# Kernel optimization log

Measured on AMD Instinct MI355X. Metric: run time of the kernel, lower is better.

Reference implementation:

```python
import jax, jax.numpy as jnp
import numpy as np

B, T, D, H = 1, 2048, 1024, 16
HS = D // H  # 64
FF = 4 * D   # 4096
EPS = 1e-6


def rmsnorm(x, w):
    xf = x.astype(jnp.float32)
    n = xf * jax.lax.rsqrt(jnp.mean(xf * xf, axis=-1, keepdims=True) + EPS)
    return n.astype(x.dtype) * w


def setup_inputs() -> dict:
    key = jax.random.key(0)
    ks = jax.random.split(key, 9)
    s = 0.02
    return {
        "x": jax.random.normal(ks[0], (B, T, D), jnp.float32),
        "Wq": jax.random.normal(ks[1], (H, D, HS), jnp.float32) * s,
        "Wk": jax.random.normal(ks[2], (H, D, HS), jnp.float32) * s,
        "Wv": jax.random.normal(ks[3], (H, D, HS), jnp.float32) * s,
        "Wproj": jax.random.normal(ks[4], (H * HS, D), jnp.float32) * s,
        "bproj": jnp.zeros((D,), jnp.float32),
        "W1": jax.random.normal(ks[5], (D, FF), jnp.float32) * s,
        "W2": jax.random.normal(ks[6], (FF, D), jnp.float32) * s,
        "g1": jnp.ones((D,), jnp.float32),
        "g2": jnp.ones((D,), jnp.float32),
    }


def reference(x, Wq, Wk, Wv, Wproj, bproj, W1, W2, g1, g2):
    # --- self attention on RMSNorm(x) ---
    xn = rmsnorm(x, g1)                                   # [B,T,D]
    q = jnp.einsum('btd,hds->bhts', xn, Wq)               # [B,H,T,hs]
    k = jnp.einsum('btd,hds->bhts', xn, Wk)
    v = jnp.einsum('btd,hds->bhts', xn, Wv)
    scale = HS ** -0.5
    wei = jnp.einsum('bhts,bhus->bhtu', q, k) * scale     # [B,H,T,T]
    causal = jnp.tril(jnp.ones((T, T), bool))
    wei = jnp.where(causal, wei, -jnp.inf)
    wei = jax.nn.softmax(wei, axis=-1)
    attn = jnp.einsum('bhtu,bhus->bhts', wei, v)          # [B,H,T,hs]
    attn = attn.transpose(0, 2, 1, 3).reshape(B, T, H * HS)
    sa = attn @ Wproj + bproj                             # [B,T,D]
    x = x + sa
    # --- SiLU FFN on RMSNorm(x) ---
    xn2 = rmsnorm(x, g2)
    h = jax.nn.silu(xn2 @ W1)                             # [B,T,4D]
    x = x + h @ W2
    return x
```

## Files before the change

### kernel.cpp

```cpp
#include <hip/hip_runtime.h>

typedef unsigned short u16;
typedef unsigned int u32;
typedef __attribute__((ext_vector_type(4))) float f32x4;
typedef __attribute__((ext_vector_type(8))) __bf16 bf16x8;

#define T_SEQ 2048
#define DMODEL 1024
#define NHEAD 16
#define HEADS 64
#define FFDIM 4096
#define MNQ 2097152l

__device__ __forceinline__ u16 f2bf(float f) {
  u32 u = __builtin_bit_cast(u32, f);
  u = u + 0x7FFFu + ((u >> 16) & 1u);
  return (u16)(u >> 16);
}
__device__ __forceinline__ float bf2f(u16 h) {
  u32 u = ((u32)h) << 16;
  return __builtin_bit_cast(float, u);
}
__device__ __forceinline__ void gload_lds16(const u16* g, u16* l) {
  __builtin_amdgcn_global_load_lds(
      (const __attribute__((address_space(1))) u32*)g,
      (__attribute__((address_space(3))) u32*)l, 16, 0, 0);
}

__device__ __forceinline__ void transpose64(const float* __restrict__ in,
                                            long ldin, u16* __restrict__ out,
                                            long ldout, int r0, int c0, int tid,
                                            u16* tile) {
#pragma unroll
  for (int p = 0; p < 4; ++p) {
    int idx = p * 256 + tid;
    int r = idx >> 4, c4 = (idx & 15) * 4;
    float4 v = *(const float4*)(in + (long)(r0 + r) * ldin + c0 + c4);
    tile[(c4 + 0) * 66 + r] = f2bf(v.x);
    tile[(c4 + 1) * 66 + r] = f2bf(v.y);
    tile[(c4 + 2) * 66 + r] = f2bf(v.z);
    tile[(c4 + 3) * 66 + r] = f2bf(v.w);
  }
  __syncthreads();
#pragma unroll
  for (int p = 0; p < 2; ++p) {
    int idx = p * 256 + tid;
    int c = idx >> 3, rg = (idx & 7) * 8;
    u16 tmp[8];
#pragma unroll
    for (int j = 0; j < 8; ++j) tmp[j] = tile[c * 66 + rg + j];
    *(uint4*)(out + (long)(c0 + c) * ldout + r0 + rg) = *(uint4*)tmp;
  }
}

__global__ __launch_bounds__(256) void prep_k(
    const float* __restrict__ Wq, const float* __restrict__ Wk,
    const float* __restrict__ Wv, const float* __restrict__ Wproj,
    const float* __restrict__ x, const float* __restrict__ g1,
    u16* __restrict__ QKVwT, u16* __restrict__ WprojT, u16* __restrict__ xn1) {
  __shared__ u16 tile[64 * 66];
  __shared__ float wsum[4];
  int bid = blockIdx.x;
  int tid = threadIdx.x;
  if (bid >= 1024) {
    int row = bid - 1024;
    const float4* xr = (const float4*)(x + (long)row * DMODEL);
    float4 v = xr[tid];
    float ss = v.x * v.x + v.y * v.y + v.z * v.z + v.w * v.w;
#pragma unroll
    for (int off = 32; off >= 1; off >>= 1) ss += __shfl_xor(ss, off, 64);
    if ((tid & 63) == 0) wsum[tid >> 6] = ss;
    __syncthreads();
    float tot = wsum[0] + wsum[1] + wsum[2] + wsum[3];
    float rms = rsqrtf(tot * (1.0f / DMODEL) + 1e-6f);
    float4 gv = ((const float4*)g1)[tid];
    ushort4 o4 = make_ushort4(f2bf(v.x * rms * gv.x), f2bf(v.y * rms * gv.y),
                              f2bf(v.z * rms * gv.z), f2bf(v.w * rms * gv.w));
    ((ushort4*)(xn1 + (long)row * DMODEL))[tid] = o4;
    return;
  }
  const float* in;
  u16* out;
  long ldin, ldout;
  int r0, c0;
  if (bid < 768) {
    int z = bid >> 4, xi = bid & 15;
    int wsel = z >> 4, h = z & 15;
    in = (wsel == 0 ? Wq : (wsel == 1 ? Wk : Wv)) + (long)h * 65536;
    out = QKVwT + (long)wsel * 1048576 + (long)h * 65536;
    ldin = 64; ldout = 1024;
    r0 = xi * 64; c0 = 0;
  } else {
    int b = bid - 768;
    in = Wproj; out = WprojT; ldin = 1024; ldout = 1024;
    r0 = (b >> 4) * 64; c0 = (b & 15) * 64;
  }
  transpose64(in, ldin, out, ldout, r0, c0, tid, tile);
}

__global__ __launch_bounds__(256) void proj_rms_k(
    const u16* __restrict__ part, const float* __restrict__ bias,
    const float* __restrict__ resid, const float* __restrict__ g,
    float* __restrict__ x1, u16* __restrict__ xn2) {
  int row = blockIdx.x;
  int tid = threadIdx.x;
  long i = (long)row * DMODEL + tid * 4;
  float4 r = *(const float4*)(resid + i);
  float4 bi = *(const float4*)(bias + tid * 4);
  float4 v;
  v.x = r.x + bi.x; v.y = r.y + bi.y; v.z = r.z + bi.z; v.w = r.w + bi.w;
#pragma unroll
  for (int z = 0; z < 2; ++z) {
    ushort4 a = *(const ushort4*)(part + z * MNQ + i);
    v.x += bf2f(a.x); v.y += bf2f(a.y); v.z += bf2f(a.z); v.w += bf2f(a.w);
  }
  *(float4*)(x1 + i) = v;
  float ss = v.x * v.x + v.y * v.y + v.z * v.z + v.w * v.w;
#pragma unroll
  for (int off = 32; off >= 1; off >>= 1) ss += __shfl_xor(ss, off, 64);
  __shared__ float wsum[4];
  if ((tid & 63) == 0) wsum[tid >> 6] = ss;
  __syncthreads();
  float tot = wsum[0] + wsum[1] + wsum[2] + wsum[3];
  float rms = rsqrtf(tot * (1.0f / DMODEL) + 1e-6f);
  float4 gv = ((const float4*)g)[tid];
  ushort4 o4 = make_ushort4(f2bf(v.x * rms * gv.x), f2bf(v.y * rms * gv.y),
                            f2bf(v.z * rms * gv.z), f2bf(v.w * rms * gv.w));
  ((ushort4*)(xn2 + (long)row * DMODEL))[tid] = o4;
}

template <int EPI, int MODE, int NITER, bool FILL = false>
__global__ __launch_bounds__(256, 3) void gemm_bt_k(
    const u16* __restrict__ A, const u16* __restrict__ Bt, int N,
    u16* __restrict__ out16, u16* __restrict__ vt,
    u16* __restrict__ p0, u16* __restrict__ p1,
    const float* __restrict__ F1, const float* __restrict__ F2,
    u16* __restrict__ FT1, u16* __restrict__ FT2, int ngemm) {
  __shared__ __align__(16) u16 As[3][128 * 32];
  __shared__ __align__(16) u16 Bs[3][128 * 32];
  if constexpr (FILL) {
    if ((int)blockIdx.x >= ngemm) {
      int tb = (int)blockIdx.x - ngemm;
      u16* tile = (u16*)As;
      const float* in;
      u16* out;
      long ldin, ldout;
      int r0, c0;
      if (tb < 1024) {
        in = F1; out = FT1; ldin = 4096; ldout = 1024;
        r0 = (tb & 15) * 64; c0 = (tb >> 4) * 64;
      } else {
        int b = tb - 1024;
        in = F2; out = FT2; ldin = 1024; ldout = 4096;
        r0 = (b >> 4) * 64; c0 = (b & 15) * 64;
      }
      transpose64(in, ldin, out, ldout, r0, c0, threadIdx.x, tile);
      return;
    }
  }
  const int K = 1024;
  const int kc = NITER * 32;
  int tid = threadIdx.x;
  int w = tid >> 6, lane = tid & 63;
  int quad = lane >> 4, l15 = lane & 15;
  int wr = w >> 1, wc = w & 1;

  int bid = blockIdx.x;
  int xcd = bid & 7, s = bid >> 3;
  int nn = N >> 7;
  int bx, by, kz;
  {
    int nl = nn >> 3;
    by = xcd * nl + s % nl;
    int r = s / nl;
    bx = r & 15;
    kz = r >> 4;
  }
  int m0 = bx * 128, n0 = by * 128;

  f32x4 acc[4][4] = {};

  int lr = lane >> 2;
  int sw = (lr >> 1) & 3;
  int lc = ((lane & 3) ^ sw) * 8;
  const u16* Ak = A + (long)(m0 + w * 32 + lr) * K + lc + (long)kz * kc;
  const u16* A2k = Ak + (long)16 * K;
  const u16* Bk = Bt + (long)(n0 + w * 32 + lr) * K + lc + (long)kz * kc;
  const u16* B2k = Bk + (long)16 * K;

  gload_lds16(Ak, As[0] + w * 1024);
  gload_lds16(A2k, As[0] + w * 1024 + 512);
  gload_lds16(Bk, Bs[0] + w * 1024);
  gload_lds16(B2k, Bs[0] + w * 1024 + 512);
  gload_lds16(Ak + 32, As[1] + w * 1024);
  gload_lds16(A2k + 32, As[1] + w * 1024 + 512);
  gload_lds16(Bk + 32, Bs[1] + w * 1024);
  gload_lds16(B2k + 32, Bs[1] + w * 1024 + 512);

  int swq = (l15 >> 1) & 3;
  int qoff = (quad ^ swq) << 3;

#pragma unroll
  for (int k = 0; k < NITER; ++k) {
    const int cb = k % 3;
    if (k + 2 < NITER) {
      asm volatile("s_waitcnt vmcnt(4)\n\ts_barrier" ::: "memory");
      const int pb = (k + 2) % 3;
      const int off = (k + 2) * 32;
      gload_lds16(Ak + off, As[pb] + w * 1024);
      gload_lds16(A2k + off, As[pb] + w * 1024 + 512);
      gload_lds16(Bk + off, Bs[pb] + w * 1024);
      gload_lds16(B2k + off, Bs[pb] + w * 1024 + 512);
    } else {
      asm volatile("s_waitcnt vmcnt(0)\n\ts_barrier" ::: "memory");
    }
    const u16* Ab = As[cb];
    const u16* Bb = Bs[cb];
    bf16x8 af[4], bfr[4];
#pragma unroll
    for (int mt = 0; mt < 4; ++mt)
      af[mt] = *(const bf16x8*)(Ab + (wr * 64 + mt * 16 + l15) * 32 + qoff);
#pragma unroll
    for (int nt = 0; nt < 4; ++nt)
      bfr[nt] = *(const bf16x8*)(Bb + (wc * 64 + nt * 16 + l15) * 32 + qoff);
#pragma unroll
    for (int mt = 0; mt < 4; ++mt)
#pragma unroll
      for (int nt = 0; nt < 4; ++nt)
        acc[mt][nt] = __builtin_amdgcn_mfma_f32_16x16x32_bf16(
            af[mt], bfr[nt], acc[mt][nt], 0, 0, 0);
  }

  bool vblock = (EPI == 0) && (vt != nullptr) && (n0 >= 2048);
  u16* pb = nullptr;
  if (EPI == 4) pb = p0 + (long)kz * MNQ;
#pragma unroll
  for (int mt = 0; mt < 4; ++mt)
#pragma unroll
    for (int nt = 0; nt < 4; ++nt) {
      int col = n0 + wc * 64 + nt * 16 + l15;
      if (EPI == 0 && vblock) {
        int sc = col - 2048;
        int row0 = m0 + wr * 64 + mt * 16 + quad * 4;
        ushort4 pk = make_ushort4(f2bf(acc[mt][nt][0]), f2bf(acc[mt][nt][1]),
                                  f2bf(acc[mt][nt][2]), f2bf(acc[mt][nt][3]));
        *(ushort4*)(vt + (long)sc * 2048 + row0) = pk;
        continue;
      }
#pragma unroll
      for (int r = 0; r < 4; ++r) {
        int row = m0 + wr * 64 + mt * 16 + quad * 4 + r;
        long idx = (long)row * N + col;
        float v = acc[mt][nt][r];
        if (EPI == 0) {
          out16[idx] = f2bf(v);
        } else if (EPI == 4) {
          pb[idx] = f2bf(v);
        }
      }
    }
}

template <int EPI, int NITER>
__global__ __launch_bounds__(256, 2) void gemm_wide_k(
    const u16* __restrict__ A, const u16* __restrict__ Bt,
    u16* __restrict__ out16, u16* __restrict__ p0, u16* __restrict__ p1) {
  __shared__ __align__(16) u16 As[3][128 * 32];
  __shared__ __align__(16) u16 Bs[3][256 * 32];
  const int K = (EPI == 4) ? 4096 : 1024;
  const int N = (EPI == 4) ? 1024 : 4096;
  const int kc = NITER * 32;
  int tid = threadIdx.x;
  int w = tid >> 6, lane = tid & 63;
  int quad = lane >> 4, l15 = lane & 15;
  int wr = w >> 1, wc = w & 1;

  int bid = blockIdx.x;
  int xcd = bid & 7, s = bid >> 3;
  int bx, by, kz;
  if (EPI == 2) {
    by = xcd * 2 + (s & 1);
    bx = s >> 1;
    kz = 0;
  } else {
    kz = xcd;
    by = s & 3;
    bx = s >> 2;
  }
  int m0 = bx * 128, n0 = by * 256;

  f32x4 acc[4][8] = {};

  int lr = lane >> 2;
  int sw = (lr >> 1) & 3;
  int lc = ((lane & 3) ^ sw) * 8;
  const u16* Ak = A + (long)(m0 + w * 32 + lr) * K + (long)kz * kc + lc;
  const u16* A2k = Ak + (long)16 * K;
  const u16* Bk0 = Bt + (long)(n0 + w * 64 + lr) * K + (long)kz * kc + lc;
  const u16* Bk1 = Bk0 + (long)16 * K;
  const u16* Bk2 = Bk0 + (long)32 * K;
  const u16* Bk3 = Bk0 + (long)48 * K;

#pragma unroll
  for (int t = 0; t < 2; ++t) {
    const int off = t * 32;
    gload_lds16(Ak + off, As[t] + w * 1024);
    gload_lds16(A2k + off, As[t] + w * 1024 + 512);
    gload_lds16(Bk0 + off, Bs[t] + w * 2048);
    gload_lds16(Bk1 + off, Bs[t] + w * 2048 + 512);
    gload_lds16(Bk2 + off, Bs[t] + w * 2048 + 1024);
    gload_lds16(Bk3 + off, Bs[t] + w * 2048 + 1536);
  }

  int swq = (l15 >> 1) & 3;
  int qoff = (quad ^ swq) << 3;

#pragma unroll
  for (int k = 0; k < NITER; ++k) {
    const int cb = k % 3;
    if (k + 2 < NITER) {
      asm volatile("s_waitcnt vmcnt(6)\n\ts_barrier" ::: "memory");
      const int pb2 = (k + 2) % 3;
      const int off = (k + 2) * 32;
      gload_lds16(Ak + off, As[pb2] + w * 1024);
      gload_lds16(A2k + off, As[pb2] + w * 1024 + 512);
      gload_lds16(Bk0 + off, Bs[pb2] + w * 2048);
      gload_lds16(Bk1 + off, Bs[pb2] + w * 2048 + 512);
      gload_lds16(Bk2 + off, Bs[pb2] + w * 2048 + 1024);
      gload_lds16(Bk3 + off, Bs[pb2] + w * 2048 + 1536);
    } else if (k + 2 == NITER) {
      asm volatile("s_waitcnt vmcnt(6)\n\ts_barrier" ::: "memory");
    } else {
      asm volatile("s_waitcnt vmcnt(0)\n\ts_barrier" ::: "memory");
    }
    const u16* Ab = As[cb];
    const u16* Bb = Bs[cb];
    bf16x8 af[4], bfr[8];
#pragma unroll
    for (int mt = 0; mt < 4; ++mt)
      af[mt] = *(const bf16x8*)(Ab + (wr * 64 + mt * 16 + l15) * 32 + qoff);
#pragma unroll
    for (int nt = 0; nt < 8; ++nt)
      bfr[nt] = *(const bf16x8*)(Bb + (wc * 128 + nt * 16 + l15) * 32 + qoff);
#pragma unroll
    for (int mt = 0; mt < 4; ++mt)
#pragma unroll
      for (int nt = 0; nt < 8; ++nt)
        acc[mt][nt] = __builtin_amdgcn_mfma_f32_16x16x32_bf16(
            af[mt], bfr[nt], acc[mt][nt], 0, 0, 0);
  }

  u16* pb = nullptr;
  if (EPI == 4)
    pb = (kz < 4) ? (p0 + (long)kz * MNQ) : (p1 + (long)(kz - 4) * MNQ);
#pragma unroll
  for (int mt = 0; mt < 4; ++mt)
#pragma unroll
    for (int nt = 0; nt < 8; ++nt) {
      int col = n0 + wc * 128 + nt * 16 + l15;
#pragma unroll
      for (int r = 0; r < 4; ++r) {
        int row = m0 + wr * 64 + mt * 16 + quad * 4 + r;
        float v = acc[mt][nt][r];
        if (EPI == 2) {
          out16[(long)row * N + col] = f2bf(v / (1.0f + __expf(-v)));
        } else {
          pb[(long)row * N + col] = f2bf(v);
        }
      }
    }
}

__global__ __launch_bounds__(256) void reduce_ffn2_k(
    const u16* __restrict__ p0, const u16* __restrict__ p1,
    const float* __restrict__ resid, float* __restrict__ out) {
  long i = ((long)blockIdx.x * 256 + threadIdx.x) * 4;
  float4 r = *(const float4*)(resid + i);
  float4 o = r;
#pragma unroll
  for (int z = 0; z < 4; ++z) {
    ushort4 a = *(const ushort4*)(p0 + z * MNQ + i);
    ushort4 b = *(const ushort4*)(p1 + z * MNQ + i);
    o.x += bf2f(a.x) + bf2f(b.x);
    o.y += bf2f(a.y) + bf2f(b.y);
    o.z += bf2f(a.z) + bf2f(b.z);
    o.w += bf2f(a.w) + bf2f(b.w);
  }
  *(float4*)(out + i) = o;
}

#define LSTR 72
__global__ __launch_bounds__(256) void attn_part_k(const u16* __restrict__ QKV,
                                                   const u16* __restrict__ Vt,
                                                   u16* __restrict__ Opart,
                                                   float* __restrict__ lpart,
                                                   u16* __restrict__ attn) {
  __shared__ __align__(16) u16 Qs[64 * LSTR];
  __shared__ __align__(16) u16 Ks[64 * LSTR];
  __shared__ __align__(16) u16 Vs[64 * LSTR];
  __shared__ float lbuf[64];

  int tid = threadIdx.x;
  int w = tid >> 6, lane = tid & 63;
  int quad = lane >> 4, l15 = lane & 15;

  int bid = blockIdx.x;
  int xcd = bid & 7, sg = bid >> 3;
  int h = xcd * 2 + (sg & 1);
  int p = sg >> 1;

  int bx = 0, acc0 = 0;
  while (true) {
    int n = (bx >> 3) + 1;
    if (p < acc0 + n) break;
    acc0 += n;
    ++bx;
  }
  int c = p - acc0;
  int t0 = bx * 64;
  int jstart = c * 8;
  int jend = min(jstart + 8, bx + 1);

#pragma unroll
  for (int pp = 0; pp < 2; ++pp) {
    int idx = pp * 256 + tid;
    int row = idx >> 3, cc = idx & 7;
    *(uint4*)(Qs + row * LSTR + cc * 8) =
        *(const uint4*)(QKV + (long)(t0 + row) * 3072 + h * 64 + cc * 8);
  }
  __syncthreads();
  bf16x8 aq[2];
#pragma unroll
  for (int ks = 0; ks < 2; ++ks)
    aq[ks] = *(const bf16x8*)(Qs + (w * 16 + l15) * LSTR + ks * 32 + quad * 8);

  f32x4 oacc[4] = {};
  float lsum = 0.f;
  int qg = t0 + w * 16 + l15;

  u16* PsW = Qs + w * (16 * LSTR);

  for (int j = jstart; j < jend; ++j) {
    __syncthreads();
#pragma unroll
    for (int pp = 0; pp < 2; ++pp) {
      int idx = pp * 256 + tid;
      int row = idx >> 3, cc = idx & 7;
      *(uint4*)(Ks + row * LSTR + cc * 8) =
          *(const uint4*)(QKV + (long)(j * 64 + row) * 3072 + 1024 + h * 64 + cc * 8);
      *(uint4*)(Vs + row * LSTR + cc * 8) =
          *(const uint4*)(Vt + (long)h * (64 * 2048) + (long)row * 2048 + j * 64 + cc * 8);
    }
    __syncthreads();

    f32x4 sacc[4] = {};
#pragma unroll
    for (int ks = 0; ks < 2; ++ks)
#pragma unroll
      for (int ut = 0; ut < 4; ++ut) {
        bf16x8 kf = *(const bf16x8*)(Ks + (ut * 16 + l15) * LSTR + ks * 32 + quad * 8);
        sacc[ut] = __builtin_amdgcn_mfma_f32_16x16x32_bf16(kf, aq[ks], sacc[ut], 0, 0, 0);
      }

    bool boundary = (j == bx);
#pragma unroll
    for (int ut = 0; ut < 4; ++ut) {
      float pv[4];
#pragma unroll
      for (int r = 0; r < 4; ++r) {
        float v = exp2f(sacc[ut][r] * 0.18033688f);
        if (boundary) {
          int u = j * 64 + ut * 16 + quad * 4 + r;
          if (u > qg) v = 0.f;
        }
        pv[r] = v;
        lsum += v;
      }
      ushort4 pk = make_ushort4(f2bf(pv[0]), f2bf(pv[1]), f2bf(pv[2]), f2bf(pv[3]));
      *(ushort4*)(PsW + l15 * LSTR + ut * 16 + quad * 4) = pk;
    }
    asm volatile("s_waitcnt lgkmcnt(0)" ::: "memory");
#pragma unroll
    for (int ks = 0; ks < 2; ++ks) {
      bf16x8 pf = *(const bf16x8*)(PsW + l15 * LSTR + ks * 32 + quad * 8);
#pragma unroll
      for (int ct = 0; ct < 4; ++ct) {
        bf16x8 vf = *(const bf16x8*)(Vs + (ct * 16 + l15) * LSTR + ks * 32 + quad * 8);
        oacc[ct] = __builtin_amdgcn_mfma_f32_16x16x32_bf16(pf, vf, oacc[ct], 0, 0, 0);
      }
    }
  }

  lsum += __shfl_xor(lsum, 16, 64);
  lsum += __shfl_xor(lsum, 32, 64);
  if (quad == 0) lbuf[w * 16 + l15] = 1.0f / lsum;
  asm volatile("s_waitcnt lgkmcnt(0)" ::: "memory");

  float inv[4];
#pragma unroll
  for (int r = 0; r < 4; ++r) inv[r] = lbuf[w * 16 + quad * 4 + r];

  if (bx < 8) {
#pragma unroll
    for (int ct = 0; ct < 4; ++ct)
#pragma unroll
      for (int r = 0; r < 4; ++r)
        attn[(long)(t0 + w * 16 + quad * 4 + r) * 1024 + h * 64 + ct * 16 + l15] =
            f2bf(oacc[ct][r] * inv[r]);
    return;
  }
  long slot = (long)p * 16 + h;
  u16* Ob = Opart + slot * 4096;
#pragma unroll
  for (int ct = 0; ct < 4; ++ct)
#pragma unroll
    for (int r = 0; r < 4; ++r)
      Ob[(w * 16 + quad * 4 + r) * 64 + ct * 16 + l15] = f2bf(oacc[ct][r] * inv[r]);
  if (quad == 0) lpart[slot * 64 + w * 16 + l15] = lsum;
}

__global__ __launch_bounds__(256) void attn_combine_k(
    const u16* __restrict__ Opart, const float* __restrict__ lpart,
    u16* __restrict__ out) {
  int bx = blockIdx.x + 8, h = blockIdx.y;
  int g = bx >> 3;
  int p0 = 4 * g * (g + 1) + (bx - 8 * g) * (g + 1);
  int nc = g + 1;
  int tid = threadIdx.x;
  int row = tid >> 2, c4 = (tid & 3) * 16;

  float lv[4];
  float wsum = 0.f;
  for (int cidx = 0; cidx < nc; ++cidx) {
    long slot = (long)(p0 + cidx) * 16 + h;
    lv[cidx] = lpart[slot * 64 + row];
    wsum += lv[cidx];
  }
  float rinv = 1.0f / wsum;

  float o[16];
#pragma unroll
  for (int i = 0; i < 16; ++i) o[i] = 0.f;
  for (int cidx = 0; cidx < nc; ++cidx) {
    float wc = lv[cidx] * rinv;
    const u16* Ob = Opart + ((long)(p0 + cidx) * 16 + h) * 4096 + row * 64 + c4;
    bf16x8 a = *(const bf16x8*)Ob;
    bf16x8 b = *(const bf16x8*)(Ob + 8);
#pragma unroll
    for (int i = 0; i < 8; ++i) {
      o[i] += wc * (float)a[i];
      o[8 + i] += wc * (float)b[i];
    }
  }
  u16 ob[16];
#pragma unroll
  for (int i = 0; i < 16; ++i) ob[i] = f2bf(o[i]);
  u16* op = out + (long)(bx * 64 + row) * 1024 + h * 64 + c4;
  *(uint4*)op = *(uint4*)ob;
  *(uint4*)(op + 8) = *(uint4*)(ob + 8);
}

extern "C" void kernel_launch(void* const* d_in, const int* in_sizes, int n_in,
                              void* d_out, int out_size, void* d_ws, size_t ws_size,
                              hipStream_t stream) {
  const float* x     = (const float*)d_in[0];
  const float* Wq    = (const float*)d_in[1];
  const float* Wk    = (const float*)d_in[2];
  const float* Wv    = (const float*)d_in[3];
  const float* Wproj = (const float*)d_in[4];
  const float* bproj = (const float*)d_in[5];
  const float* W1    = (const float*)d_in[6];
  const float* W2    = (const float*)d_in[7];
  const float* g1    = (const float*)d_in[8];
  const float* g2    = (const float*)d_in[9];

  char* ws = (char*)d_ws;
  u16* QKVwT  = (u16*)(ws);
  u16* WprojT = (u16*)(ws + (6ul << 20));
  u16* W1T    = (u16*)(ws + (8ul << 20));
  u16* W2T    = (u16*)(ws + (16ul << 20));
  u16* xn1    = (u16*)(ws + (24ul << 20));
  u16* QKVb   = (u16*)(ws + (28ul << 20));
  u16* VtB    = (u16*)(ws + (40ul << 20));
  u16* attn   = (u16*)(ws + (44ul << 20));
  float* x1   = (float*)(ws + (48ul << 20));
  u16* xn2    = (u16*)(ws + (56ul << 20));
  u16* hbuf   = (u16*)(ws + (60ul << 20));
  u16* Opart    = (u16*)(ws + (48ul << 20));
  float* lpart  = (float*)(ws + (58ul << 20));
  u16* projp    = (u16*)(ws + (28ul << 20));
  u16* ffn2pA   = (u16*)(ws + (28ul << 20));
  u16* ffn2pB   = (u16*)(ws);
  if (ws_size < (76ul << 20)) return;

  dim3 blk(256);

  prep_k<<<dim3(3072), blk, 0, stream>>>(
      Wq, Wk, Wv, Wproj, x, g1, QKVwT, WprojT, xn1);
  gemm_bt_k<0, 0, 32, true><<<dim3(2432), blk, 0, stream>>>(
      xn1, QKVwT, 3072, QKVb, VtB, nullptr, nullptr, W1, W2, W1T, W2T, 384);
  attn_part_k<<<dim3(1280), blk, 0, stream>>>(QKVb, VtB, Opart, lpart, attn);
  attn_combine_k<<<dim3(24, 16), blk, 0, stream>>>(Opart, lpart, attn);
  gemm_bt_k<4, 0, 16><<<dim3(256), blk, 0, stream>>>(
      attn, WprojT, 1024, nullptr, nullptr, projp, nullptr,
      nullptr, nullptr, nullptr, nullptr, 0);
  proj_rms_k<<<dim3(2048), blk, 0, stream>>>(projp, bproj, x, g2, x1, xn2);
  gemm_wide_k<2, 32><<<dim3(256), blk, 0, stream>>>(
      xn2, W1T, hbuf, nullptr, nullptr);
  gemm_wide_k<4, 16><<<dim3(512), blk, 0, stream>>>(
      hbuf, W2T, nullptr, ffn2pA, ffn2pB);
  reduce_ffn2_k<<<dim3(2048), blk, 0, stream>>>(ffn2pA, ffn2pB, x1, (float*)d_out);
}
```

Before: 243.8 us.

## Move Wproj transpose into QKV fill, prefetch attention K/V, split proj GEMM 4-way

Moves the Wproj transpose out of the prep kernel and into the fill blocks of the QKV GEMM, so it overlaps with GEMM work and the prep grid shrinks. The attention kernel now loads the next K/V tile into registers while computing the current one, hiding global load latency at the cost of extra registers. The projection GEMM uses a smaller K chunk with twice the blocks (4-way split-K), and the proj_rms reduction sums 4 partials. The extra partials add memory traffic in exchange for more parallelism.

```diff
diff --git a/kernel.cpp b/kernel.cpp
--- a/kernel.cpp
+++ b/kernel.cpp
@@ -55,15 +55,15 @@
 
 __global__ __launch_bounds__(256) void prep_k(
     const float* __restrict__ Wq, const float* __restrict__ Wk,
-    const float* __restrict__ Wv, const float* __restrict__ Wproj,
-    const float* __restrict__ x, const float* __restrict__ g1,
-    u16* __restrict__ QKVwT, u16* __restrict__ WprojT, u16* __restrict__ xn1) {
+    const float* __restrict__ Wv, const float* __restrict__ x,
+    const float* __restrict__ g1, u16* __restrict__ QKVwT,
+    u16* __restrict__ xn1) {
   __shared__ u16 tile[64 * 66];
   __shared__ float wsum[4];
   int bid = blockIdx.x;
   int tid = threadIdx.x;
-  if (bid >= 1024) {
-    int row = bid - 1024;
+  if (bid >= 768) {
+    int row = bid - 768;
     const float4* xr = (const float4*)(x + (long)row * DMODEL);
     float4 v = xr[tid];
     float ss = v.x * v.x + v.y * v.y + v.z * v.z + v.w * v.w;
@@ -79,23 +79,11 @@
     ((ushort4*)(xn1 + (long)row * DMODEL))[tid] = o4;
     return;
   }
-  const float* in;
-  u16* out;
-  long ldin, ldout;
-  int r0, c0;
-  if (bid < 768) {
-    int z = bid >> 4, xi = bid & 15;
-    int wsel = z >> 4, h = z & 15;
-    in = (wsel == 0 ? Wq : (wsel == 1 ? Wk : Wv)) + (long)h * 65536;
-    out = QKVwT + (long)wsel * 1048576 + (long)h * 65536;
-    ldin = 64; ldout = 1024;
-    r0 = xi * 64; c0 = 0;
-  } else {
-    int b = bid - 768;
-    in = Wproj; out = WprojT; ldin = 1024; ldout = 1024;
-    r0 = (b >> 4) * 64; c0 = (b & 15) * 64;
-  }
-  transpose64(in, ldin, out, ldout, r0, c0, tid, tile);
+  int z = bid >> 4, xi = bid & 15;
+  int wsel = z >> 4, h = z & 15;
+  const float* in = (wsel == 0 ? Wq : (wsel == 1 ? Wk : Wv)) + (long)h * 65536;
+  u16* out = QKVwT + (long)wsel * 1048576 + (long)h * 65536;
+  transpose64(in, 64, out, 1024, xi * 64, 0, tid, tile);
 }
 
 __global__ __launch_bounds__(256) void proj_rms_k(
@@ -110,7 +98,7 @@
   float4 v;
   v.x = r.x + bi.x; v.y = r.y + bi.y; v.z = r.z + bi.z; v.w = r.w + bi.w;
 #pragma unroll
-  for (int z = 0; z < 2; ++z) {
+  for (int z = 0; z < 4; ++z) {
     ushort4 a = *(const ushort4*)(part + z * MNQ + i);
     v.x += bf2f(a.x); v.y += bf2f(a.y); v.z += bf2f(a.z); v.w += bf2f(a.w);
   }
@@ -135,7 +123,8 @@
     u16* __restrict__ out16, u16* __restrict__ vt,
     u16* __restrict__ p0, u16* __restrict__ p1,
     const float* __restrict__ F1, const float* __restrict__ F2,
-    u16* __restrict__ FT1, u16* __restrict__ FT2, int ngemm) {
+    const float* __restrict__ F3, u16* __restrict__ FT1,
+    u16* __restrict__ FT2, u16* __restrict__ FT3, int ngemm) {
   __shared__ __align__(16) u16 As[3][128 * 32];
   __shared__ __align__(16) u16 Bs[3][128 * 32];
   if constexpr (FILL) {
@@ -149,9 +138,13 @@
       if (tb < 1024) {
         in = F1; out = FT1; ldin = 4096; ldout = 1024;
         r0 = (tb & 15) * 64; c0 = (tb >> 4) * 64;
-      } else {
+      } else if (tb < 2048) {
         int b = tb - 1024;
         in = F2; out = FT2; ldin = 1024; ldout = 4096;
+        r0 = (b >> 4) * 64; c0 = (b & 15) * 64;
+      } else {
+        int b = tb - 2048;
+        in = F3; out = FT3; ldin = 1024; ldout = 1024;
         r0 = (b >> 4) * 64; c0 = (b & 15) * 64;
       }
       transpose64(in, ldin, out, ldout, r0, c0, threadIdx.x, tile);
@@ -421,6 +414,15 @@
   int jstart = c * 8;
   int jend = min(jstart + 8, bx + 1);
 
+  int srow0 = tid >> 3, scc = (tid & 7) * 8;
+  int srow1 = srow0 + 32;
+
+  uint4 kN[2], vN[2];
+  kN[0] = *(const uint4*)(QKV + (long)(jstart * 64 + srow0) * 3072 + 1024 + h * 64 + scc);
+  kN[1] = *(const uint4*)(QKV + (long)(jstart * 64 + srow1) * 3072 + 1024 + h * 64 + scc);
+  vN[0] = *(const uint4*)(Vt + (long)h * (64 * 2048) + (long)srow0 * 2048 + jstart * 64 + scc);
+  vN[1] = *(const uint4*)(Vt + (long)h * (64 * 2048) + (long)srow1 * 2048 + jstart * 64 + scc);
+
 #pragma unroll
   for (int pp = 0; pp < 2; ++pp) {
     int idx = pp * 256 + tid;
@@ -442,14 +444,16 @@
 
   for (int j = jstart; j < jend; ++j) {
     __syncthreads();
-#pragma unroll
-    for (int pp = 0; pp < 2; ++pp) {
-      int idx = pp * 256 + tid;
-      int row = idx >> 3, cc = idx & 7;
-      *(uint4*)(Ks + row * LSTR + cc * 8) =
-          *(const uint4*)(QKV + (long)(j * 64 + row) * 3072 + 1024 + h * 64 + cc * 8);
-      *(uint4*)(Vs + row * LSTR + cc * 8) =
-          *(const uint4*)(Vt + (long)h * (64 * 2048) + (long)row * 2048 + j * 64 + cc * 8);
+    *(uint4*)(Ks + srow0 * LSTR + scc) = kN[0];
+    *(uint4*)(Ks + srow1 * LSTR + scc) = kN[1];
+    *(uint4*)(Vs + srow0 * LSTR + scc) = vN[0];
+    *(uint4*)(Vs + srow1 * LSTR + scc) = vN[1];
+    if (j + 1 < jend) {
+      int jn = j + 1;
+      kN[0] = *(const uint4*)(QKV + (long)(jn * 64 + srow0) * 3072 + 1024 + h * 64 + scc);
+      kN[1] = *(const uint4*)(QKV + (long)(jn * 64 + srow1) * 3072 + 1024 + h * 64 + scc);
+      vN[0] = *(const uint4*)(Vt + (long)h * (64 * 2048) + (long)srow0 * 2048 + jn * 64 + scc);
+      vN[1] = *(const uint4*)(Vt + (long)h * (64 * 2048) + (long)srow1 * 2048 + jn * 64 + scc);
     }
     __syncthreads();
 
@@ -595,15 +599,15 @@
 
   dim3 blk(256);
 
-  prep_k<<<dim3(3072), blk, 0, stream>>>(
-      Wq, Wk, Wv, Wproj, x, g1, QKVwT, WprojT, xn1);
-  gemm_bt_k<0, 0, 32, true><<<dim3(2432), blk, 0, stream>>>(
-      xn1, QKVwT, 3072, QKVb, VtB, nullptr, nullptr, W1, W2, W1T, W2T, 384);
+  prep_k<<<dim3(2816), blk, 0, stream>>>(Wq, Wk, Wv, x, g1, QKVwT, xn1);
+  gemm_bt_k<0, 0, 32, true><<<dim3(2688), blk, 0, stream>>>(
+      xn1, QKVwT, 3072, QKVb, VtB, nullptr, nullptr,
+      W1, W2, Wproj, W1T, W2T, WprojT, 384);
   attn_part_k<<<dim3(1280), blk, 0, stream>>>(QKVb, VtB, Opart, lpart, attn);
   attn_combine_k<<<dim3(24, 16), blk, 0, stream>>>(Opart, lpart, attn);
-  gemm_bt_k<4, 0, 16><<<dim3(256), blk, 0, stream>>>(
+  gemm_bt_k<4, 0, 8><<<dim3(512), blk, 0, stream>>>(
       attn, WprojT, 1024, nullptr, nullptr, projp, nullptr,
-      nullptr, nullptr, nullptr, nullptr, 0);
+      nullptr, nullptr, nullptr, nullptr, nullptr, nullptr, 0);
   proj_rms_k<<<dim3(2048), blk, 0, stream>>>(projp, bproj, x, g2, x1, xn2);
   gemm_wide_k<2, 32><<<dim3(256), blk, 0, stream>>>(
       xn2, W1T, hbuf, nullptr, nullptr);
```

Result: slower. 278.5 us (+14.2%).
